# Optimization experiments

Measured on AMD Instinct MI355X. Metric: run time of the kernel, lower is better.

## Reference

```python
import jax, jax.numpy as jnp
import numpy as np

N_NODES = 50000
N_EDGES = 400000
D_IN = 512
D_OUT = 512


def setup_inputs() -> dict:
    key = jax.random.key(0)
    k1, k2, k3, k4, k5 = jax.random.split(key, 5)
    x = jax.random.normal(k1, (N_NODES, D_IN), dtype=jnp.float32)
    adj_rows = jax.random.randint(k2, (N_EDGES,), 0, N_NODES, dtype=jnp.int32)
    adj_cols = jax.random.randint(k3, (N_EDGES,), 0, N_NODES, dtype=jnp.int32)
    adj_vals = jax.random.uniform(k4, (N_EDGES,), dtype=jnp.float32)
    # Xavier uniform init for weight, zeros for bias (as in reset_parameters)
    limit = float(np.sqrt(6.0 / (D_IN + D_OUT)))
    weight = jax.random.uniform(k5, (D_IN, D_OUT), minval=-limit, maxval=limit, dtype=jnp.float32)
    bias = jnp.zeros((D_OUT,), dtype=jnp.float32)
    return {"x": x, "adj_rows": adj_rows, "adj_cols": adj_cols,
            "adj_vals": adj_vals, "weight": weight, "bias": bias}


def reference(x, adj_rows, adj_cols, adj_vals, weight, bias):
    # support = x @ W  : dense GEMM [N, D_in] x [D_in, D_out]
    support = jnp.matmul(x, weight)
    # output = spmm(adj, support): COO sparse-dense matmul via gather + segment_sum
    messages = adj_vals[:, None] * support[adj_cols]  # [E, D_out]
    output = jax.ops.segment_sum(messages, adj_rows, num_segments=N_NODES)
    return output + bias
```

## Files before the change

kernel.cpp:

```cpp
#include <hip/hip_runtime.h>

#define N_NODES 50000
#define N_EDGES 400000
#define DIM 512
#define NPAD 50048
#define MTILES 391
#define NTILES 4
#define NWG (MTILES * NTILES)

typedef short  short8  __attribute__((ext_vector_type(8)));
typedef unsigned short ushort8 __attribute__((ext_vector_type(8)));
typedef float  f32x4   __attribute__((ext_vector_type(4)));
typedef int    int2v   __attribute__((ext_vector_type(2)));

typedef __attribute__((address_space(1))) const unsigned short gu16;
typedef __attribute__((address_space(3))) unsigned short lu16;

__device__ __forceinline__ unsigned short f2bf(float f) {
    unsigned int u = __float_as_uint(f);
    u += 0x7fffu + ((u >> 16) & 1u);
    return (unsigned short)(u >> 16);
}
__device__ __forceinline__ float bf2f(unsigned short h) {
    return __uint_as_float(((unsigned int)h) << 16);
}

__global__ __launch_bounds__(256) void cast_x_kernel(const float* __restrict__ x,
                                                     unsigned short* __restrict__ xb) {
    size_t t = (size_t)blockIdx.x * 256 + threadIdx.x;
    size_t base = t * 8;
    int row = (int)(base >> 9);
    ushort8 o;
    if (row < N_NODES) {
        f32x4 a = *(const f32x4*)(x + base);
        f32x4 b = *(const f32x4*)(x + base + 4);
        o[0] = f2bf(a[0]); o[1] = f2bf(a[1]); o[2] = f2bf(a[2]); o[3] = f2bf(a[3]);
        o[4] = f2bf(b[0]); o[5] = f2bf(b[1]); o[6] = f2bf(b[2]); o[7] = f2bf(b[3]);
    } else {
        #pragma unroll
        for (int q = 0; q < 8; ++q) o[q] = 0;
    }
    *(ushort8*)(xb + base) = o;
}

__global__ __launch_bounds__(256) void wt_hist_kernel(const float* __restrict__ w,
                                                      unsigned short* __restrict__ wt,
                                                      const int* __restrict__ rows,
                                                      int* __restrict__ counts) {
    int b = blockIdx.x;
    if (b < 1024) {
        int t = b * 256 + threadIdx.x;
        int n = t >> 9, k = t & 511;
        wt[t] = f2bf(w[k * 512 + n]);
    } else {
        int e = (b - 1024) * 256 + threadIdx.x;
        if (e < N_EDGES) atomicAdd(&counts[rows[e]], 1);
    }
}

__global__ __launch_bounds__(512) void scan_blocks_kernel(const int* __restrict__ counts,
                                                          int* __restrict__ tmp,
                                                          int* __restrict__ partials) {
    __shared__ int sm[512];
    int i = blockIdx.x * 512 + threadIdx.x;
    int v = (i < N_NODES) ? counts[i] : 0;
    sm[threadIdx.x] = v;
    __syncthreads();
    #pragma unroll
    for (int off = 1; off < 512; off <<= 1) {
        int val = 0;
        if ((int)threadIdx.x >= off) val = sm[threadIdx.x - off];
        __syncthreads();
        if ((int)threadIdx.x >= off) sm[threadIdx.x] += val;
        __syncthreads();
    }
    if (i < N_NODES) tmp[i] = sm[threadIdx.x] - v;
    if (threadIdx.x == 511) partials[blockIdx.x] = sm[511];
}

__global__ __launch_bounds__(128) void scan_partials_kernel(int* __restrict__ partials) {
    __shared__ int sm[128];
    const int nb = 98;
    int v = ((int)threadIdx.x < nb) ? partials[threadIdx.x] : 0;
    sm[threadIdx.x] = v;
    __syncthreads();
    #pragma unroll
    for (int off = 1; off < 128; off <<= 1) {
        int val = 0;
        if ((int)threadIdx.x >= off) val = sm[threadIdx.x - off];
        __syncthreads();
        if ((int)threadIdx.x >= off) sm[threadIdx.x] += val;
        __syncthreads();
    }
    if ((int)threadIdx.x < nb) partials[threadIdx.x] = sm[threadIdx.x] - v;
}

__global__ __launch_bounds__(256) void add_offsets_kernel(const int* __restrict__ tmp,
                                                          const int* __restrict__ partials,
                                                          int* __restrict__ row_start,
                                                          int* __restrict__ cursor) {
    int i = blockIdx.x * 256 + threadIdx.x;
    if (i < N_NODES) {
        int rs = tmp[i] + partials[i >> 9];
        row_start[i] = rs;
        cursor[i] = rs;
    }
}

__global__ __launch_bounds__(256) void scatter_kernel(const int* __restrict__ rows,
                                                      const int* __restrict__ cols,
                                                      const float* __restrict__ vals,
                                                      int* __restrict__ cursor,
                                                      int2v* __restrict__ csr_cv) {
    int e = blockIdx.x * 256 + threadIdx.x;
    if (e < N_EDGES) {
        int r = rows[e];
        int p = atomicAdd(&cursor[r], 1);
        int2v cv;
        cv[0] = cols[e];
        cv[1] = __float_as_int(vals[e]);
        csr_cv[p] = cv;
    }
}

__global__ __launch_bounds__(256) void gemm_kernel(const unsigned short* __restrict__ Xb,
                                                   const unsigned short* __restrict__ Wt,
                                                   unsigned short* __restrict__ S) {
    __shared__ __align__(16) unsigned short As[128 * 64];
    __shared__ __align__(16) unsigned short Bs[128 * 64];

    const int q = NWG / 8, r8 = NWG % 8;
    int b = blockIdx.x;
    int xcd = b & 7, loc = b >> 3;
    int l = (xcd < r8 ? xcd * (q + 1) : r8 * (q + 1) + (xcd - r8) * q) + loc;
    const int m0 = (l >> 2) * 128;
    const int n0 = (l & 3) * 128;

    const int t = threadIdx.x;
    const int lane = t & 63;
    const int w = t >> 6;
    const int wr = w >> 1, wc = w & 1;
    const int fr = lane & 15;
    const int kg = lane >> 4;

    f32x4 acc[4][4];
    #pragma unroll
    for (int i = 0; i < 4; ++i)
        #pragma unroll
        for (int j = 0; j < 4; ++j)
            #pragma unroll
            for (int qq = 0; qq < 4; ++qq) acc[i][j][qq] = 0.0f;

    const int srow = w * 8 + (lane >> 3);
    const int scol = (lane & 7) * 8;
    const unsigned short* gA = Xb + (size_t)(m0 + srow) * DIM + scol;
    const unsigned short* gB = Wt + (size_t)(n0 + srow) * DIM + scol;
    lu16* AsW = (lu16*)As + w * 512;
    lu16* BsW = (lu16*)Bs + w * 512;

    for (int kk = 0; kk < DIM; kk += 64) {
        #pragma unroll
        for (int c = 0; c < 4; ++c) {
            __builtin_amdgcn_global_load_lds((gu16*)(gA + (size_t)c * 32 * DIM + kk), AsW + c * 2048, 16, 0, 0);
            __builtin_amdgcn_global_load_lds((gu16*)(gB + (size_t)c * 32 * DIM + kk), BsW + c * 2048, 16, 0, 0);
        }
        __syncthreads();

        short8 af[4][2], bf[4][2];
        #pragma unroll
        for (int mi = 0; mi < 4; ++mi)
            #pragma unroll
            for (int ks = 0; ks < 2; ++ks)
                af[mi][ks] = *(const short8*)&As[(wr * 64 + mi * 16 + fr) * 64 + ks * 32 + kg * 8];
        #pragma unroll
        for (int ni = 0; ni < 4; ++ni)
            #pragma unroll
            for (int ks = 0; ks < 2; ++ks)
                bf[ni][ks] = *(const short8*)&Bs[(wc * 64 + ni * 16 + fr) * 64 + ks * 32 + kg * 8];

        #pragma unroll
        for (int ks = 0; ks < 2; ++ks)
            #pragma unroll
            for (int mi = 0; mi < 4; ++mi)
                #pragma unroll
                for (int ni = 0; ni < 4; ++ni)
                    acc[mi][ni] = __builtin_amdgcn_mfma_f32_16x16x32_bf16(af[mi][ks], bf[ni][ks], acc[mi][ni], 0, 0, 0);

        __syncthreads();
    }

    #pragma unroll
    for (int mi = 0; mi < 4; ++mi) {
        #pragma unroll
        for (int ni = 0; ni < 4; ++ni) {
            int gr = m0 + wr * 64 + mi * 16 + kg * 4;
            int gc = n0 + wc * 64 + ni * 16 + fr;
            #pragma unroll
            for (int j = 0; j < 4; ++j)
                S[(size_t)(gr + j) * DIM + gc] = f2bf(acc[mi][ni][j]);
        }
    }
}

__global__ __launch_bounds__(256) void spmm_kernel(const unsigned short* __restrict__ S,
                                                   const int* __restrict__ row_start,
                                                   const int* __restrict__ counts,
                                                   const int2v* __restrict__ cv,
                                                   const float* __restrict__ bias,
                                                   float* __restrict__ out) {
    const int r = blockIdx.x * 4 + (threadIdx.x >> 6);
    const int lane = threadIdx.x & 63;
    const int s = row_start[r];
    const int n = counts[r];
    const size_t lo = (size_t)lane * 8;

    float acc[8];
    #pragma unroll
    for (int q = 0; q < 8; ++q) acc[q] = 0.0f;

    for (int j = 0; j < n; j += 4) {
        int2v e0 = cv[s + j];
        int2v e1 = cv[s + j + 1];
        int2v e2 = cv[s + j + 2];
        int2v e3 = cv[s + j + 3];
        int c0 = e0[0];
        int c1 = (j + 1 < n) ? e1[0] : 0;
        int c2 = (j + 2 < n) ? e2[0] : 0;
        int c3 = (j + 3 < n) ? e3[0] : 0;
        float v0 = __int_as_float(e0[1]);
        float v1 = (j + 1 < n) ? __int_as_float(e1[1]) : 0.0f;
        float v2 = (j + 2 < n) ? __int_as_float(e2[1]) : 0.0f;
        float v3 = (j + 3 < n) ? __int_as_float(e3[1]) : 0.0f;
        ushort8 x0 = *(const ushort8*)&S[(size_t)c0 * DIM + lo];
        ushort8 x1 = *(const ushort8*)&S[(size_t)c1 * DIM + lo];
        ushort8 x2 = *(const ushort8*)&S[(size_t)c2 * DIM + lo];
        ushort8 x3 = *(const ushort8*)&S[(size_t)c3 * DIM + lo];
        #pragma unroll
        for (int q = 0; q < 8; ++q) {
            acc[q] += v0 * bf2f(x0[q]);
            acc[q] += v1 * bf2f(x1[q]);
            acc[q] += v2 * bf2f(x2[q]);
            acc[q] += v3 * bf2f(x3[q]);
        }
    }

    #pragma unroll
    for (int q = 0; q < 8; ++q) acc[q] += bias[lane * 8 + q];

    f32x4 o0, o1;
    #pragma unroll
    for (int q = 0; q < 4; ++q) { o0[q] = acc[q]; o1[q] = acc[4 + q]; }
    *(f32x4*)&out[(size_t)r * DIM + lo] = o0;
    *(f32x4*)&out[(size_t)r * DIM + lo + 4] = o1;
}

extern "C" void kernel_launch(void* const* d_in, const int* in_sizes, int n_in,
                              void* d_out, int out_size, void* d_ws, size_t ws_size,
                              hipStream_t stream) {
    const float* x    = (const float*)d_in[0];
    const int*   rows = (const int*)d_in[1];
    const int*   cols = (const int*)d_in[2];
    const float* vals = (const float*)d_in[3];
    const float* w    = (const float*)d_in[4];
    const float* bias = (const float*)d_in[5];
    float* out = (float*)d_out;

    char* ws = (char*)d_ws;
    size_t off = 0;
    auto alloc = [&](size_t bytes) -> char* {
        char* p = ws + off;
        off = (off + bytes + 255) & ~(size_t)255;
        return p;
    };
    unsigned short* Xb      = (unsigned short*)alloc((size_t)NPAD * DIM * 2);
    unsigned short* Wt      = (unsigned short*)alloc((size_t)DIM * DIM * 2);
    unsigned short* S       = (unsigned short*)alloc((size_t)NPAD * DIM * 2);
    int*            counts  = (int*)alloc((size_t)N_NODES * 4);
    int*            tmp     = (int*)alloc((size_t)N_NODES * 4);
    int*            rstart  = (int*)alloc((size_t)N_NODES * 4);
    int*            cursor  = (int*)alloc((size_t)N_NODES * 4);
    int*            partials= (int*)alloc(512);
    int2v*          csr_cv  = (int2v*)alloc((size_t)(N_EDGES + 8) * 8);

    hipMemsetAsync(counts, 0, (size_t)N_NODES * 4, stream);

    cast_x_kernel<<<(NPAD * DIM / 8) / 256, 256, 0, stream>>>(x, Xb);
    wt_hist_kernel<<<1024 + (N_EDGES + 255) / 256, 256, 0, stream>>>(w, Wt, rows, counts);

    scan_blocks_kernel<<<98, 512, 0, stream>>>(counts, tmp, partials);
    scan_partials_kernel<<<1, 128, 0, stream>>>(partials);
    add_offsets_kernel<<<(N_NODES + 255) / 256, 256, 0, stream>>>(tmp, partials, rstart, cursor);
    scatter_kernel<<<(N_EDGES + 255) / 256, 256, 0, stream>>>(rows, cols, vals, cursor, csr_cv);

    gemm_kernel<<<NWG, 256, 0, stream>>>(Xb, Wt, S);
    spmm_kernel<<<N_NODES / 4, 256, 0, stream>>>(S, rstart, counts, csr_cv, bias, out);
}
```

Baseline: 348.1 us.

## Split SpMM into two column-half passes with 4-wide gathers

The SpMM now runs as two launches, each covering half of the 512 output columns, with each lane gathering 4 bf16 values (8 bytes) instead of 8. The aim is to shrink the working set of S touched per pass so more of it stays in cache, and to reduce register pressure. In exchange, the CSR index and value arrays are read twice, gathers are narrower, and there is an extra launch.

After: 354.0 us. No clear change (+1.7%).

```diff
diff --git a/kernel.cpp b/kernel.cpp
--- a/kernel.cpp
+++ b/kernel.cpp
@@ -10,6 +10,7 @@
 
 typedef short  short8  __attribute__((ext_vector_type(8)));
 typedef unsigned short ushort8 __attribute__((ext_vector_type(8)));
+typedef unsigned short ushort4v __attribute__((ext_vector_type(4)));
 typedef float  f32x4   __attribute__((ext_vector_type(4)));
 typedef int    int2v   __attribute__((ext_vector_type(2)));
 
@@ -207,16 +208,16 @@
                                                    const int* __restrict__ counts,
                                                    const int2v* __restrict__ cv,
                                                    const float* __restrict__ bias,
-                                                   float* __restrict__ out) {
+                                                   float* __restrict__ out,
+                                                   int d0) {
     const int r = blockIdx.x * 4 + (threadIdx.x >> 6);
     const int lane = threadIdx.x & 63;
     const int s = row_start[r];
     const int n = counts[r];
-    const size_t lo = (size_t)lane * 8;
-
-    float acc[8];
-    #pragma unroll
-    for (int q = 0; q < 8; ++q) acc[q] = 0.0f;
+    const int d = d0 + lane * 4;
+    const unsigned short* Sd = S + d;
+
+    float a0 = 0.f, a1 = 0.f, a2 = 0.f, a3 = 0.f;
 
     for (int j = 0; j < n; j += 4) {
         int2v e0 = cv[s + j];
@@ -231,27 +232,22 @@
         float v1 = (j + 1 < n) ? __int_as_float(e1[1]) : 0.0f;
         float v2 = (j + 2 < n) ? __int_as_float(e2[1]) : 0.0f;
         float v3 = (j + 3 < n) ? __int_as_float(e3[1]) : 0.0f;
-        ushort8 x0 = *(const ushort8*)&S[(size_t)c0 * DIM + lo];
-        ushort8 x1 = *(const ushort8*)&S[(size_t)c1 * DIM + lo];
-        ushort8 x2 = *(const ushort8*)&S[(size_t)c2 * DIM + lo];
-        ushort8 x3 = *(const ushort8*)&S[(size_t)c3 * DIM + lo];
-        #pragma unroll
-        for (int q = 0; q < 8; ++q) {
-            acc[q] += v0 * bf2f(x0[q]);
-            acc[q] += v1 * bf2f(x1[q]);
-            acc[q] += v2 * bf2f(x2[q]);
-            acc[q] += v3 * bf2f(x3[q]);
-        }
-    }
-
-    #pragma unroll
-    for (int q = 0; q < 8; ++q) acc[q] += bias[lane * 8 + q];
-
-    f32x4 o0, o1;
-    #pragma unroll
-    for (int q = 0; q < 4; ++q) { o0[q] = acc[q]; o1[q] = acc[4 + q]; }
-    *(f32x4*)&out[(size_t)r * DIM + lo] = o0;
-    *(f32x4*)&out[(size_t)r * DIM + lo + 4] = o1;
+        ushort4v x0 = *(const ushort4v*)&Sd[(size_t)c0 * DIM];
+        ushort4v x1 = *(const ushort4v*)&Sd[(size_t)c1 * DIM];
+        ushort4v x2 = *(const ushort4v*)&Sd[(size_t)c2 * DIM];
+        ushort4v x3 = *(const ushort4v*)&Sd[(size_t)c3 * DIM];
+        a0 += v0 * bf2f(x0[0]) + v1 * bf2f(x1[0]) + v2 * bf2f(x2[0]) + v3 * bf2f(x3[0]);
+        a1 += v0 * bf2f(x0[1]) + v1 * bf2f(x1[1]) + v2 * bf2f(x2[1]) + v3 * bf2f(x3[1]);
+        a2 += v0 * bf2f(x0[2]) + v1 * bf2f(x1[2]) + v2 * bf2f(x2[2]) + v3 * bf2f(x3[2]);
+        a3 += v0 * bf2f(x0[3]) + v1 * bf2f(x1[3]) + v2 * bf2f(x2[3]) + v3 * bf2f(x3[3]);
+    }
+
+    f32x4 o;
+    o[0] = a0 + bias[d];
+    o[1] = a1 + bias[d + 1];
+    o[2] = a2 + bias[d + 2];
+    o[3] = a3 + bias[d + 3];
+    *(f32x4*)&out[(size_t)r * DIM + d] = o;
 }
 
 extern "C" void kernel_launch(void* const* d_in, const int* in_sizes, int n_in,
@@ -293,5 +289,6 @@
     scatter_kernel<<<(N_EDGES + 255) / 256, 256, 0, stream>>>(rows, cols, vals, cursor, csr_cv);
 
     gemm_kernel<<<NWG, 256, 0, stream>>>(Xb, Wt, S);
-    spmm_kernel<<<N_NODES / 4, 256, 0, stream>>>(S, rstart, counts, csr_cv, bias, out);
-}
+    spmm_kernel<<<N_NODES / 4, 256, 0, stream>>>(S, rstart, counts, csr_cv, bias, out, 0);
+    spmm_kernel<<<N_NODES / 4, 256, 0, stream>>>(S, rstart, counts, csr_cv, bias, out, 256);
+}
```

## Fuse prep kernels, fold partial scan into offsets, unroll SpMM gather by eight

Applied to the files above, without the earlier changes.

Merges the x-cast kernel with the weight-transpose and histogram kernel into one launch. Folds the single-block partials scan into add_offsets_kernel, where every block redundantly rescans the 98 partials. Widens the SpMM edge loop from 4 to 8 edges per iteration so more independent gathers are in flight. Together these cut two kernel launches and their serialization gaps and aim for more memory-level parallelism in the gather, at the cost of redundant scan work per block and higher register use in SpMM. With an average of 8 edges per row, the wider unroll also means more masked-off loads on rows with fewer edges.

After: 340.3 us. -2.2%, faster.

```diff
diff --git a/kernel.cpp b/kernel.cpp
--- a/kernel.cpp
+++ b/kernel.cpp
@@ -8,6 +8,10 @@
 #define NTILES 4
 #define NWG (MTILES * NTILES)
 
+#define PREP_XBLK 12512
+#define PREP_WBLK 1024
+#define PREP_HBLK 1563
+
 typedef short  short8  __attribute__((ext_vector_type(8)));
 typedef unsigned short ushort8 __attribute__((ext_vector_type(8)));
 typedef float  f32x4   __attribute__((ext_vector_type(4)));
@@ -25,35 +29,34 @@
     return __uint_as_float(((unsigned int)h) << 16);
 }
 
-__global__ __launch_bounds__(256) void cast_x_kernel(const float* __restrict__ x,
-                                                     unsigned short* __restrict__ xb) {
-    size_t t = (size_t)blockIdx.x * 256 + threadIdx.x;
-    size_t base = t * 8;
-    int row = (int)(base >> 9);
-    ushort8 o;
-    if (row < N_NODES) {
-        f32x4 a = *(const f32x4*)(x + base);
-        f32x4 b = *(const f32x4*)(x + base + 4);
-        o[0] = f2bf(a[0]); o[1] = f2bf(a[1]); o[2] = f2bf(a[2]); o[3] = f2bf(a[3]);
-        o[4] = f2bf(b[0]); o[5] = f2bf(b[1]); o[6] = f2bf(b[2]); o[7] = f2bf(b[3]);
-    } else {
-        #pragma unroll
-        for (int q = 0; q < 8; ++q) o[q] = 0;
-    }
-    *(ushort8*)(xb + base) = o;
-}
-
-__global__ __launch_bounds__(256) void wt_hist_kernel(const float* __restrict__ w,
-                                                      unsigned short* __restrict__ wt,
-                                                      const int* __restrict__ rows,
-                                                      int* __restrict__ counts) {
+__global__ __launch_bounds__(256) void prep_kernel(const float* __restrict__ x,
+                                                   unsigned short* __restrict__ xb,
+                                                   const float* __restrict__ w,
+                                                   unsigned short* __restrict__ wt,
+                                                   const int* __restrict__ rows,
+                                                   int* __restrict__ counts) {
     int b = blockIdx.x;
-    if (b < 1024) {
-        int t = b * 256 + threadIdx.x;
+    if (b < PREP_XBLK) {
+        size_t t = (size_t)b * 256 + threadIdx.x;
+        size_t base = t * 8;
+        int row = (int)(base >> 9);
+        ushort8 o;
+        if (row < N_NODES) {
+            f32x4 a = *(const f32x4*)(x + base);
+            f32x4 c = *(const f32x4*)(x + base + 4);
+            o[0] = f2bf(a[0]); o[1] = f2bf(a[1]); o[2] = f2bf(a[2]); o[3] = f2bf(a[3]);
+            o[4] = f2bf(c[0]); o[5] = f2bf(c[1]); o[6] = f2bf(c[2]); o[7] = f2bf(c[3]);
+        } else {
+            #pragma unroll
+            for (int q = 0; q < 8; ++q) o[q] = 0;
+        }
+        *(ushort8*)(xb + base) = o;
+    } else if (b < PREP_XBLK + PREP_WBLK) {
+        int t = (b - PREP_XBLK) * 256 + threadIdx.x;
         int n = t >> 9, k = t & 511;
         wt[t] = f2bf(w[k * 512 + n]);
     } else {
-        int e = (b - 1024) * 256 + threadIdx.x;
+        int e = (b - PREP_XBLK - PREP_WBLK) * 256 + threadIdx.x;
         if (e < N_EDGES) atomicAdd(&counts[rows[e]], 1);
     }
 }
@@ -78,30 +81,32 @@
     if (threadIdx.x == 511) partials[blockIdx.x] = sm[511];
 }
 
-__global__ __launch_bounds__(128) void scan_partials_kernel(int* __restrict__ partials) {
-    __shared__ int sm[128];
-    const int nb = 98;
-    int v = ((int)threadIdx.x < nb) ? partials[threadIdx.x] : 0;
-    sm[threadIdx.x] = v;
-    __syncthreads();
-    #pragma unroll
-    for (int off = 1; off < 128; off <<= 1) {
-        int val = 0;
-        if ((int)threadIdx.x >= off) val = sm[threadIdx.x - off];
-        __syncthreads();
-        if ((int)threadIdx.x >= off) sm[threadIdx.x] += val;
-        __syncthreads();
-    }
-    if ((int)threadIdx.x < nb) partials[threadIdx.x] = sm[threadIdx.x] - v;
-}
-
 __global__ __launch_bounds__(256) void add_offsets_kernel(const int* __restrict__ tmp,
                                                           const int* __restrict__ partials,
                                                           int* __restrict__ row_start,
                                                           int* __restrict__ cursor) {
-    int i = blockIdx.x * 256 + threadIdx.x;
+    __shared__ int pin[128], pinc[128];
+    const int tid = threadIdx.x;
+    const int nb = 98;
+    if (tid < 128) {
+        int v = (tid < nb) ? partials[tid] : 0;
+        pin[tid] = v;
+        pinc[tid] = v;
+    }
+    __syncthreads();
+    #pragma unroll
+    for (int off = 1; off < 128; off <<= 1) {
+        int val = 0;
+        if (tid < 128 && tid >= off) val = pinc[tid - off];
+        __syncthreads();
+        if (tid < 128 && tid >= off) pinc[tid] += val;
+        __syncthreads();
+    }
+    int i = blockIdx.x * 256 + tid;
     if (i < N_NODES) {
-        int rs = tmp[i] + partials[i >> 9];
+        int b9 = i >> 9;
+        int excl = pinc[b9] - pin[b9];
+        int rs = tmp[i] + excl;
         row_start[i] = rs;
         cursor[i] = rs;
     }
@@ -218,30 +223,25 @@
     #pragma unroll
     for (int q = 0; q < 8; ++q) acc[q] = 0.0f;
 
-    for (int j = 0; j < n; j += 4) {
-        int2v e0 = cv[s + j];
-        int2v e1 = cv[s + j + 1];
-        int2v e2 = cv[s + j + 2];
-        int2v e3 = cv[s + j + 3];
-        int c0 = e0[0];
-        int c1 = (j + 1 < n) ? e1[0] : 0;
-        int c2 = (j + 2 < n) ? e2[0] : 0;
-        int c3 = (j + 3 < n) ? e3[0] : 0;
-        float v0 = __int_as_float(e0[1]);
-        float v1 = (j + 1 < n) ? __int_as_float(e1[1]) : 0.0f;
-        float v2 = (j + 2 < n) ? __int_as_float(e2[1]) : 0.0f;
-        float v3 = (j + 3 < n) ? __int_as_float(e3[1]) : 0.0f;
-        ushort8 x0 = *(const ushort8*)&S[(size_t)c0 * DIM + lo];
-        ushort8 x1 = *(const ushort8*)&S[(size_t)c1 * DIM + lo];
-        ushort8 x2 = *(const ushort8*)&S[(size_t)c2 * DIM + lo];
-        ushort8 x3 = *(const ushort8*)&S[(size_t)c3 * DIM + lo];
-        #pragma unroll
-        for (int q = 0; q < 8; ++q) {
-            acc[q] += v0 * bf2f(x0[q]);
-            acc[q] += v1 * bf2f(x1[q]);
-            acc[q] += v2 * bf2f(x2[q]);
-            acc[q] += v3 * bf2f(x3[q]);
-        }
+    for (int j = 0; j < n; j += 8) {
+        int   cc[8];
+        float vv[8];
+        #pragma unroll
+        for (int k = 0; k < 8; ++k) {
+            int2v e = cv[s + j + k];
+            bool ok = (j + k < n);
+            cc[k] = ok ? e[0] : 0;
+            vv[k] = ok ? __int_as_float(e[1]) : 0.0f;
+        }
+        ushort8 xv[8];
+        #pragma unroll
+        for (int k = 0; k < 8; ++k)
+            xv[k] = *(const ushort8*)&S[(size_t)cc[k] * DIM + lo];
+        #pragma unroll
+        for (int k = 0; k < 8; ++k)
+            #pragma unroll
+            for (int q = 0; q < 8; ++q)
+                acc[q] += vv[k] * bf2f(xv[k][q]);
     }
 
     #pragma unroll
@@ -284,11 +284,8 @@
 
     hipMemsetAsync(counts, 0, (size_t)N_NODES * 4, stream);
 
-    cast_x_kernel<<<(NPAD * DIM / 8) / 256, 256, 0, stream>>>(x, Xb);
-    wt_hist_kernel<<<1024 + (N_EDGES + 255) / 256, 256, 0, stream>>>(w, Wt, rows, counts);
-
+    prep_kernel<<<PREP_XBLK + PREP_WBLK + PREP_HBLK, 256, 0, stream>>>(x, Xb, w, Wt, rows, counts);
     scan_blocks_kernel<<<98, 512, 0, stream>>>(counts, tmp, partials);
-    scan_partials_kernel<<<1, 128, 0, stream>>>(partials);
     add_offsets_kernel<<<(N_NODES + 255) / 256, 256, 0, stream>>>(tmp, partials, rstart, cursor);
     scatter_kernel<<<(N_EDGES + 255) / 256, 256, 0, stream>>>(rows, cols, vals, cursor, csr_cv);
 
```
